# Performance work log

Hardware: AMD Instinct MI355X
Metric: run time of the kernel (lower is better)

Reference implementation:

```python
import jax, jax.numpy as jnp
import numpy as np
from itertools import product

GRID = 64      # voxel grid resolution per scene
B = 8          # number of point clouds in the sparse batch
PER_B = 12500  # active voxels per scene
C = 64         # num_channels
K = 27         # 3x3x3 kernel offsets
EPS = 1e-5     # MinkowskiBatchNorm eps


def _build_kernel_map(coords):
    # coords: [N,4] int (b,x,y,z). For each of 27 offsets, find the input index
    # whose coordinate equals (b, x+dx, y+dy, z+dz); missing -> N (zero row).
    N = coords.shape[0]
    base = GRID + 2  # room for +-1 offsets after +1 shift

    def enc(b, x, y, z):
        return ((b.astype(np.int64) * base + (x + 1)) * base + (y + 1)) * base + (z + 1)

    keys = enc(coords[:, 0], coords[:, 1], coords[:, 2], coords[:, 3])
    order = np.argsort(keys)
    skeys = keys[order]
    kmap = np.full((N, K), N, dtype=np.int32)
    for k, (dx, dy, dz) in enumerate(product([-1, 0, 1], repeat=3)):
        qk = enc(coords[:, 0], coords[:, 1] + dx, coords[:, 2] + dy, coords[:, 3] + dz)
        pos = np.searchsorted(skeys, qk)
        posc = np.clip(pos, 0, N - 1)
        hit = skeys[posc] == qk
        kmap[:, k] = np.where(hit, order[posc], N)
    return kmap


def setup_inputs() -> dict:
    rng = np.random.default_rng(0)
    coords = []
    for b in range(B):
        flat = rng.choice(GRID ** 3, size=PER_B, replace=False)
        x = flat // (GRID * GRID)
        y = (flat // GRID) % GRID
        z = flat % GRID
        coords.append(np.stack([np.full(PER_B, b), x, y, z], axis=1))
    coords = np.concatenate(coords, axis=0)  # [N,4]
    kmap = _build_kernel_map(coords)         # [N,27]

    key = jax.random.key(0)
    k0, k1, k2 = jax.random.split(key, 3)
    N = coords.shape[0]
    x = jax.random.normal(k0, (N, C), dtype=jnp.float32)
    scale = 1.0 / np.sqrt(K * C)
    W1 = jax.random.normal(k1, (K, C, C), dtype=jnp.float32) * scale
    W2 = jax.random.normal(k2, (K, C, C), dtype=jnp.float32) * scale
    return {
        "x": x,
        "kmap": jnp.asarray(kmap),
        "gamma1": jnp.ones((C,), jnp.float32),
        "beta1": jnp.zeros((C,), jnp.float32),
        "W1": W1,
        "gamma2": jnp.ones((C,), jnp.float32),
        "beta2": jnp.zeros((C,), jnp.float32),
        "W2": W2,
    }


def _bn(h, gamma, beta):
    # MinkowskiBatchNorm (training mode): stats over all active points per channel
    m = h.mean(axis=0)
    v = h.var(axis=0)
    return (h - m) * jax.lax.rsqrt(v + EPS) * gamma + beta


def _sparse_conv(h, kmap, W):
    # MinkowskiConvolution stride=1: gather per-offset neighbors, GEMM, sum.
    hp = jnp.concatenate([h, jnp.zeros((1, h.shape[1]), h.dtype)], axis=0)  # zero row for misses
    g = hp[kmap]  # [N, K, C]
    return jnp.einsum('nkc,kcd->nd', g, W)


def reference(x, kmap, gamma1, beta1, W1, gamma2, beta2, W2):
    # pre-act: BN -> ReLU -> conv -> BN -> ReLU -> conv -> + residual
    out = _sparse_conv(jax.nn.relu(_bn(x, gamma1, beta1)), kmap, W1)
    out = _sparse_conv(jax.nn.relu(_bn(out, gamma2, beta2)), kmap, W2)
    return out + x
```

## Files before the change

### kernel.cpp

```cpp
#include <hip/hip_runtime.h>
#include <hip/hip_bf16.h>

#define CCH 64
#define KOFF 27
#define EPSV 1e-5f

typedef short bf16x8 __attribute__((ext_vector_type(8)));
typedef float f32x4  __attribute__((ext_vector_type(4)));

__device__ __forceinline__ void gld16(const void* g, void* l) {
    __builtin_amdgcn_global_load_lds((const __attribute__((address_space(1))) void*)g,
                                     (__attribute__((address_space(3))) void*)l, 16, 0, 0);
}

__global__ __launch_bounds__(256) void k_stats(const float* __restrict__ x, int N,
                                               float* __restrict__ sum,
                                               float* __restrict__ sumsq) {
    const int c  = threadIdx.x & 63;
    const int rg = threadIdx.x >> 6;
    float s = 0.0f, s2 = 0.0f;
    for (int r = blockIdx.x * 4 + rg; r < N; r += gridDim.x * 4) {
        float v = x[(size_t)r * CCH + c];
        s  += v;
        s2 += v * v;
    }
    __shared__ float sh[8][64];
    sh[rg][c]     = s;
    sh[4 + rg][c] = s2;
    __syncthreads();
    if (threadIdx.x < 64) {
        atomicAdd(&sum[c], sh[0][c] + sh[1][c] + sh[2][c] + sh[3][c]);
    } else if (threadIdx.x < 128) {
        const int cc = threadIdx.x - 64;
        atomicAdd(&sumsq[cc], sh[4][cc] + sh[5][cc] + sh[6][cc] + sh[7][cc]);
    }
}

__global__ __launch_bounds__(256) void k_bnrelu_bf16(const float* __restrict__ x,
                                                     const float* __restrict__ sum,
                                                     const float* __restrict__ sumsq,
                                                     const float* __restrict__ gamma,
                                                     const float* __restrict__ beta,
                                                     __hip_bfloat16* __restrict__ h,
                                                     int N) {
    const float invN = 1.0f / (float)N;
    const int total = (N + 1) * 8;
    for (int i = blockIdx.x * 256 + threadIdx.x; i < total; i += gridDim.x * 256) {
        const int r  = i >> 3;
        const int c0 = (i & 7) * 8;
        union { __hip_bfloat16 b[8]; int4 v; } pk;
        if (r < N) {
            const float4 va = ((const float4*)x)[i * 2];
            const float4 vb = ((const float4*)x)[i * 2 + 1];
            const float vv[8] = {va.x, va.y, va.z, va.w, vb.x, vb.y, vb.z, vb.w};
#pragma unroll
            for (int j = 0; j < 8; ++j) {
                const int c     = c0 + j;
                const float m   = sum[c] * invN;
                const float var = sumsq[c] * invN - m * m;
                const float sc  = gamma[c] * rsqrtf(var + EPSV);
                const float sh_ = beta[c] - m * sc;
                float t = vv[j] * sc + sh_;
                t = t > 0.0f ? t : 0.0f;
                pk.b[j] = __float2bfloat16(t);
            }
        } else {
            pk.v = make_int4(0, 0, 0, 0);
        }
        ((int4*)h)[i] = pk.v;
    }
}

__global__ __launch_bounds__(256) void k_wimg(const float* __restrict__ W1,
                                              const float* __restrict__ W2,
                                              __hip_bfloat16* __restrict__ img1,
                                              __hip_bfloat16* __restrict__ img2) {
    int k = blockIdx.x;
    const float* W = W1; __hip_bfloat16* img = img1;
    if (k >= KOFF) { k -= KOFF; W = W2; img = img2; }
    const float* src = W + (size_t)k * CCH * CCH;
    __hip_bfloat16* dst = img + (size_t)k * CCH * CCH;
    for (int e = threadIdx.x; e < CCH * CCH; e += 256) {
        const int p = e >> 3, j = e & 7;
        const int n = p >> 7, half = (p >> 6) & 1, chunk = (p >> 4) & 3, col = p & 15;
        const int c = chunk * 8 + half * 32 + j;
        const int d = n * 16 + col;
        dst[e] = __float2bfloat16(src[c * CCH + d]);
    }
}

__global__ __launch_bounds__(256) void k_conv_mfma(const __hip_bfloat16* __restrict__ h,
                                                   const int* __restrict__ kmap,
                                                   const __hip_bfloat16* __restrict__ Wimg,
                                                   const float* __restrict__ resid,
                                                   float* __restrict__ out, int N) {
    __shared__ int sidx[128 * KOFF];
    __shared__ __hip_bfloat16 wbuf[2][4096];

    const int t     = threadIdx.x;
    const int lane  = t & 63;
    const int wave  = t >> 6;
    const int col16 = lane & 15;
    const int chunk = lane >> 4;
    const int base  = blockIdx.x * 128;
    const int p0    = base + wave * 32;

    const long gbase = (long)base * KOFF;
    const long glim  = (long)N * KOFF;
    for (int j = t; j < 128 * KOFF; j += 256)
        sidx[j] = (gbase + j < glim) ? kmap[gbase + j] : N;

    {
        const __hip_bfloat16* g = Wimg + t * 8;
        gld16(g,        &wbuf[0][t * 8]);
        gld16(g + 2048, &wbuf[0][t * 8 + 2048]);
    }
    __syncthreads();

    const int r0 = wave * 32 + col16;
    const int r1 = r0 + 16;

    f32x4  acc[2][4] = {};
    bf16x8 an[2][2];

    {
        const int i0 = sidx[r0 * KOFF];
        const int i1 = sidx[r1 * KOFF];
        const bf16x8* A0 = (const bf16x8*)(h + (size_t)i0 * CCH) + chunk;
        const bf16x8* A1 = (const bf16x8*)(h + (size_t)i1 * CCH) + chunk;
        an[0][0] = A0[0]; an[0][1] = A0[4];
        an[1][0] = A1[0]; an[1][1] = A1[4];
    }

    for (int k = 0; k < KOFF; ++k) {
        if (k + 1 < KOFF) {
            const __hip_bfloat16* g = Wimg + (size_t)(k + 1) * 4096 + t * 8;
            const int nb = (k + 1) & 1;
            gld16(g,        &wbuf[nb][t * 8]);
            gld16(g + 2048, &wbuf[nb][t * 8 + 2048]);
        }
        const bf16x8 a00 = an[0][0], a01 = an[0][1], a10 = an[1][0], a11 = an[1][1];
        if (k + 1 < KOFF) {
            const int i0 = sidx[r0 * KOFF + k + 1];
            const int i1 = sidx[r1 * KOFF + k + 1];
            const bf16x8* A0 = (const bf16x8*)(h + (size_t)i0 * CCH) + chunk;
            const bf16x8* A1 = (const bf16x8*)(h + (size_t)i1 * CCH) + chunk;
            an[0][0] = A0[0]; an[0][1] = A0[4];
            an[1][0] = A1[0]; an[1][1] = A1[4];
        }
        const bf16x8* bp = (const bf16x8*)&wbuf[k & 1][0] + lane;
#pragma unroll
        for (int n = 0; n < 4; ++n) {
            const bf16x8 b0 = bp[(n * 2 + 0) * 64];
            const bf16x8 b1 = bp[(n * 2 + 1) * 64];
            acc[0][n] = __builtin_amdgcn_mfma_f32_16x16x32_bf16(a00, b0, acc[0][n], 0, 0, 0);
            acc[0][n] = __builtin_amdgcn_mfma_f32_16x16x32_bf16(a01, b1, acc[0][n], 0, 0, 0);
            acc[1][n] = __builtin_amdgcn_mfma_f32_16x16x32_bf16(a10, b0, acc[1][n], 0, 0, 0);
            acc[1][n] = __builtin_amdgcn_mfma_f32_16x16x32_bf16(a11, b1, acc[1][n], 0, 0, 0);
        }
        __syncthreads();
    }

#pragma unroll
    for (int m = 0; m < 2; ++m) {
#pragma unroll
        for (int n = 0; n < 4; ++n) {
            const int col = n * 16 + col16;
#pragma unroll
            for (int j = 0; j < 4; ++j) {
                const int row = p0 + m * 16 + chunk * 4 + j;
                if (row < N) {
                    float v = acc[m][n][j];
                    if (resid) v += resid[(size_t)row * CCH + col];
                    out[(size_t)row * CCH + col] = v;
                }
            }
        }
    }
}

extern "C" void kernel_launch(void* const* d_in, const int* in_sizes, int n_in,
                              void* d_out, int out_size, void* d_ws, size_t ws_size,
                              hipStream_t stream) {
    const float* x      = (const float*)d_in[0];
    const int*   kmap   = (const int*)d_in[1];
    const float* gamma1 = (const float*)d_in[2];
    const float* beta1  = (const float*)d_in[3];
    const float* W1     = (const float*)d_in[4];
    const float* gamma2 = (const float*)d_in[5];
    const float* beta2  = (const float*)d_in[6];
    const float* W2     = (const float*)d_in[7];
    float*       out    = (float*)d_out;

    const int N = in_sizes[0] / CCH;

    char* wp = (char*)d_ws;
    __hip_bfloat16* hbuf = (__hip_bfloat16*)wp;  wp += ((size_t)(N + 1) * CCH * 2 + 255) & ~255ull;
    __hip_bfloat16* img1 = (__hip_bfloat16*)wp;  wp += ((size_t)KOFF * CCH * CCH * 2 + 255) & ~255ull;
    __hip_bfloat16* img2 = (__hip_bfloat16*)wp;  wp += ((size_t)KOFF * CCH * CCH * 2 + 255) & ~255ull;
    float*          stats = (float*)wp;

    hipMemsetAsync(stats, 0, 256 * sizeof(float), stream);
    k_wimg<<<2 * KOFF, 256, 0, stream>>>(W1, W2, img1, img2);

    const int cgrid = (N + 127) / 128;

    k_stats      <<<304,  256, 0, stream>>>(x, N, stats + 0, stats + 64);
    k_bnrelu_bf16<<<2048, 256, 0, stream>>>(x, stats + 0, stats + 64, gamma1, beta1, hbuf, N);
    k_conv_mfma  <<<cgrid, 256, 0, stream>>>(hbuf, kmap, img1, nullptr, out, N);

    k_stats      <<<304,  256, 0, stream>>>(out, N, stats + 128, stats + 192);
    k_bnrelu_bf16<<<2048, 256, 0, stream>>>(out, stats + 128, stats + 192, gamma2, beta2, hbuf, N);
    k_conv_mfma  <<<cgrid, 256, 0, stream>>>(hbuf, kmap, img2, x, out, N);
}
```

Before: 241.3 us.

## Fuse BN stats into conv epilogue, merge weight prep with stats, halve conv tile

The second BatchNorm's per-channel sum and sum-of-squares now accumulate in the first convolution's epilogue through shared-memory atomics followed by global atomics. This removes a separate full pass over the intermediate output. The weight-image conversion and the first stats pass are merged into one launch, and the stats loop now reads float4 vectors. The conv tile shrinks from 128 to 64 rows per block, one 16-row MFMA tile per wave, which doubles the grid and halves per-wave work. The cost is more weight reloads per point and extra atomics in the epilogue.

```diff
diff --git a/kernel.cpp b/kernel.cpp
--- a/kernel.cpp
+++ b/kernel.cpp
@@ -13,26 +13,50 @@
                                      (__attribute__((address_space(3))) void*)l, 16, 0, 0);
 }
 
-__global__ __launch_bounds__(256) void k_stats(const float* __restrict__ x, int N,
-                                               float* __restrict__ sum,
-                                               float* __restrict__ sumsq) {
-    const int c  = threadIdx.x & 63;
-    const int rg = threadIdx.x >> 6;
-    float s = 0.0f, s2 = 0.0f;
-    for (int r = blockIdx.x * 4 + rg; r < N; r += gridDim.x * 4) {
-        float v = x[(size_t)r * CCH + c];
-        s  += v;
-        s2 += v * v;
-    }
-    __shared__ float sh[8][64];
-    sh[rg][c]     = s;
-    sh[4 + rg][c] = s2;
+__global__ __launch_bounds__(256) void k_pre(const float* __restrict__ W1,
+                                             const float* __restrict__ W2,
+                                             __hip_bfloat16* __restrict__ img1,
+                                             __hip_bfloat16* __restrict__ img2,
+                                             const float* __restrict__ x, int N,
+                                             float* __restrict__ sum,
+                                             float* __restrict__ sumsq) {
+    if (blockIdx.x < 2 * KOFF) {
+        int k = blockIdx.x;
+        const float* W = W1; __hip_bfloat16* img = img1;
+        if (k >= KOFF) { k -= KOFF; W = W2; img = img2; }
+        const float* src = W + (size_t)k * CCH * CCH;
+        __hip_bfloat16* dst = img + (size_t)k * CCH * CCH;
+        for (int e = threadIdx.x; e < CCH * CCH; e += 256) {
+            const int p = e >> 3, j = e & 7;
+            const int n = p >> 7, half = (p >> 6) & 1, chunk = (p >> 4) & 3, col = p & 15;
+            dst[e] = __float2bfloat16(src[(chunk * 8 + half * 32 + j) * CCH + n * 16 + col]);
+        }
+        return;
+    }
+    const int bid = blockIdx.x - 2 * KOFF;
+    const int nb  = gridDim.x - 2 * KOFF;
+    const int c4  = threadIdx.x & 15;
+    const int rg  = threadIdx.x >> 4;
+    f32x4 s = {0.f, 0.f, 0.f, 0.f}, s2 = {0.f, 0.f, 0.f, 0.f};
+    for (int r = bid * 16 + rg; r < N; r += nb * 16) {
+        const float4 v = ((const float4*)x)[(size_t)r * 16 + c4];
+        s[0] += v.x; s[1] += v.y; s[2] += v.z; s[3] += v.w;
+        s2[0] += v.x * v.x; s2[1] += v.y * v.y; s2[2] += v.z * v.z; s2[3] += v.w * v.w;
+    }
+    __shared__ float sh[2][16][64];
+#pragma unroll
+    for (int j = 0; j < 4; ++j) {
+        sh[0][rg][c4 * 4 + j] = s[j];
+        sh[1][rg][c4 * 4 + j] = s2[j];
+    }
     __syncthreads();
-    if (threadIdx.x < 64) {
-        atomicAdd(&sum[c], sh[0][c] + sh[1][c] + sh[2][c] + sh[3][c]);
-    } else if (threadIdx.x < 128) {
-        const int cc = threadIdx.x - 64;
-        atomicAdd(&sumsq[cc], sh[4][cc] + sh[5][cc] + sh[6][cc] + sh[7][cc]);
+    if (threadIdx.x < 128) {
+        const int which = threadIdx.x >> 6;
+        const int c     = threadIdx.x & 63;
+        float a = 0.f;
+#pragma unroll
+        for (int g = 0; g < 16; ++g) a += sh[which][g][c];
+        atomicAdd(which ? &sumsq[c] : &sum[c], a);
     }
 }
 
@@ -71,43 +95,28 @@
     }
 }
 
-__global__ __launch_bounds__(256) void k_wimg(const float* __restrict__ W1,
-                                              const float* __restrict__ W2,
-                                              __hip_bfloat16* __restrict__ img1,
-                                              __hip_bfloat16* __restrict__ img2) {
-    int k = blockIdx.x;
-    const float* W = W1; __hip_bfloat16* img = img1;
-    if (k >= KOFF) { k -= KOFF; W = W2; img = img2; }
-    const float* src = W + (size_t)k * CCH * CCH;
-    __hip_bfloat16* dst = img + (size_t)k * CCH * CCH;
-    for (int e = threadIdx.x; e < CCH * CCH; e += 256) {
-        const int p = e >> 3, j = e & 7;
-        const int n = p >> 7, half = (p >> 6) & 1, chunk = (p >> 4) & 3, col = p & 15;
-        const int c = chunk * 8 + half * 32 + j;
-        const int d = n * 16 + col;
-        dst[e] = __float2bfloat16(src[c * CCH + d]);
-    }
-}
-
 __global__ __launch_bounds__(256) void k_conv_mfma(const __hip_bfloat16* __restrict__ h,
                                                    const int* __restrict__ kmap,
                                                    const __hip_bfloat16* __restrict__ Wimg,
                                                    const float* __restrict__ resid,
-                                                   float* __restrict__ out, int N) {
-    __shared__ int sidx[128 * KOFF];
+                                                   float* __restrict__ out, int N,
+                                                   float* __restrict__ stat_sum,
+                                                   float* __restrict__ stat_sq) {
+    __shared__ int sidx[64 * KOFF];
     __shared__ __hip_bfloat16 wbuf[2][4096];
+    __shared__ float st[2][64];
 
     const int t     = threadIdx.x;
     const int lane  = t & 63;
     const int wave  = t >> 6;
     const int col16 = lane & 15;
     const int chunk = lane >> 4;
-    const int base  = blockIdx.x * 128;
-    const int p0    = base + wave * 32;
+    const int base  = blockIdx.x * 64;
+    const int p0    = base + wave * 16;
 
     const long gbase = (long)base * KOFF;
     const long glim  = (long)N * KOFF;
-    for (int j = t; j < 128 * KOFF; j += 256)
+    for (int j = t; j < 64 * KOFF; j += 256)
         sidx[j] = (gbase + j < glim) ? kmap[gbase + j] : N;
 
     {
@@ -117,19 +126,15 @@
     }
     __syncthreads();
 
-    const int r0 = wave * 32 + col16;
-    const int r1 = r0 + 16;
-
-    f32x4  acc[2][4] = {};
-    bf16x8 an[2][2];
+    const int r0 = wave * 16 + col16;
+
+    f32x4  acc[4] = {};
+    bf16x8 a0p, a1p;
 
     {
         const int i0 = sidx[r0 * KOFF];
-        const int i1 = sidx[r1 * KOFF];
         const bf16x8* A0 = (const bf16x8*)(h + (size_t)i0 * CCH) + chunk;
-        const bf16x8* A1 = (const bf16x8*)(h + (size_t)i1 * CCH) + chunk;
-        an[0][0] = A0[0]; an[0][1] = A0[4];
-        an[1][0] = A1[0]; an[1][1] = A1[4];
+        a0p = A0[0]; a1p = A0[4];
     }
 
     for (int k = 0; k < KOFF; ++k) {
@@ -139,43 +144,49 @@
             gld16(g,        &wbuf[nb][t * 8]);
             gld16(g + 2048, &wbuf[nb][t * 8 + 2048]);
         }
-        const bf16x8 a00 = an[0][0], a01 = an[0][1], a10 = an[1][0], a11 = an[1][1];
+        const bf16x8 a0 = a0p, a1 = a1p;
         if (k + 1 < KOFF) {
             const int i0 = sidx[r0 * KOFF + k + 1];
-            const int i1 = sidx[r1 * KOFF + k + 1];
             const bf16x8* A0 = (const bf16x8*)(h + (size_t)i0 * CCH) + chunk;
-            const bf16x8* A1 = (const bf16x8*)(h + (size_t)i1 * CCH) + chunk;
-            an[0][0] = A0[0]; an[0][1] = A0[4];
-            an[1][0] = A1[0]; an[1][1] = A1[4];
+            a0p = A0[0]; a1p = A0[4];
         }
         const bf16x8* bp = (const bf16x8*)&wbuf[k & 1][0] + lane;
 #pragma unroll
         for (int n = 0; n < 4; ++n) {
             const bf16x8 b0 = bp[(n * 2 + 0) * 64];
             const bf16x8 b1 = bp[(n * 2 + 1) * 64];
-            acc[0][n] = __builtin_amdgcn_mfma_f32_16x16x32_bf16(a00, b0, acc[0][n], 0, 0, 0);
-            acc[0][n] = __builtin_amdgcn_mfma_f32_16x16x32_bf16(a01, b1, acc[0][n], 0, 0, 0);
-            acc[1][n] = __builtin_amdgcn_mfma_f32_16x16x32_bf16(a10, b0, acc[1][n], 0, 0, 0);
-            acc[1][n] = __builtin_amdgcn_mfma_f32_16x16x32_bf16(a11, b1, acc[1][n], 0, 0, 0);
+            acc[n] = __builtin_amdgcn_mfma_f32_16x16x32_bf16(a0, b0, acc[n], 0, 0, 0);
+            acc[n] = __builtin_amdgcn_mfma_f32_16x16x32_bf16(a1, b1, acc[n], 0, 0, 0);
         }
         __syncthreads();
     }
 
-#pragma unroll
-    for (int m = 0; m < 2; ++m) {
-#pragma unroll
-        for (int n = 0; n < 4; ++n) {
-            const int col = n * 16 + col16;
-#pragma unroll
-            for (int j = 0; j < 4; ++j) {
-                const int row = p0 + m * 16 + chunk * 4 + j;
-                if (row < N) {
-                    float v = acc[m][n][j];
-                    if (resid) v += resid[(size_t)row * CCH + col];
-                    out[(size_t)row * CCH + col] = v;
-                }
+    if (stat_sum && t < 128) st[t >> 6][t & 63] = 0.0f;
+    if (stat_sum) __syncthreads();
+
+#pragma unroll
+    for (int n = 0; n < 4; ++n) {
+        const int col = n * 16 + col16;
+        float s = 0.f, s2 = 0.f;
+#pragma unroll
+        for (int j = 0; j < 4; ++j) {
+            const int row = p0 + chunk * 4 + j;
+            if (row < N) {
+                float v = acc[n][j];
+                if (resid) v += resid[(size_t)row * CCH + col];
+                out[(size_t)row * CCH + col] = v;
+                s += v; s2 += v * v;
             }
         }
+        if (stat_sum) {
+            atomicAdd(&st[0][col], s);
+            atomicAdd(&st[1][col], s2);
+        }
+    }
+    if (stat_sum) {
+        __syncthreads();
+        if (t < 64)       atomicAdd(&stat_sum[t], st[0][t]);
+        else if (t < 128) atomicAdd(&stat_sq[t - 64], st[1][t - 64]);
     }
 }
 
@@ -201,15 +212,17 @@
     float*          stats = (float*)wp;
 
     hipMemsetAsync(stats, 0, 256 * sizeof(float), stream);
-    k_wimg<<<2 * KOFF, 256, 0, stream>>>(W1, W2, img1, img2);
-
-    const int cgrid = (N + 127) / 128;
-
-    k_stats      <<<304,  256, 0, stream>>>(x, N, stats + 0, stats + 64);
+
+    k_pre<<<2 * KOFF + 512, 256, 0, stream>>>(W1, W2, img1, img2, x, N,
+                                              stats + 0, stats + 64);
+
+    const int cgrid = (N + 63) / 64;
+
     k_bnrelu_bf16<<<2048, 256, 0, stream>>>(x, stats + 0, stats + 64, gamma1, beta1, hbuf, N);
-    k_conv_mfma  <<<cgrid, 256, 0, stream>>>(hbuf, kmap, img1, nullptr, out, N);
-
-    k_stats      <<<304,  256, 0, stream>>>(out, N, stats + 128, stats + 192);
+    k_conv_mfma  <<<cgrid, 256, 0, stream>>>(hbuf, kmap, img1, nullptr, out, N,
+                                             stats + 128, stats + 192);
+
     k_bnrelu_bf16<<<2048, 256, 0, stream>>>(out, stats + 128, stats + 192, gamma2, beta2, hbuf, N);
-    k_conv_mfma  <<<cgrid, 256, 0, stream>>>(hbuf, kmap, img2, x, out, N);
-}
+    k_conv_mfma  <<<cgrid, 256, 0, stream>>>(hbuf, kmap, img2, x, out, N,
+                                             nullptr, nullptr);
+}
```

Result: slower. 255.6 us (+5.9%).
